# Kernel optimization log

Measured on AMD Instinct MI355X. Metric: run time of the kernel, lower is better.

Reference implementation:

```python
import jax, jax.numpy as jnp
import numpy as np

B, S, D = 2, 2048, 1024
H = 16
HD = D // H
E = 8          # num_experts
TOPK = 2
DF = 4 * D     # expert hidden
LN_EPS = 1e-5


def _layer_norm(h, g, b):
    mu = jnp.mean(h, axis=-1, keepdims=True)
    var = jnp.mean(jnp.square(h - mu), axis=-1, keepdims=True)
    return (h - mu) * jax.lax.rsqrt(var + LN_EPS) * g + b


def setup_inputs() -> dict:
    key = jax.random.key(0)
    ks = jax.random.split(key, 12)
    s = lambda fan: 1.0 / np.sqrt(fan)
    return {
        "x": jax.random.normal(ks[0], (B, S, D), jnp.float32),
        "ln1_g": jnp.ones((D,), jnp.float32),
        "ln1_b": jnp.zeros((D,), jnp.float32),
        "ln2_g": jnp.ones((D,), jnp.float32),
        "ln2_b": jnp.zeros((D,), jnp.float32),
        "wqkv": jax.random.normal(ks[1], (D, 3 * D), jnp.float32) * s(D),
        "bqkv": jnp.zeros((3 * D,), jnp.float32),
        "wo": jax.random.normal(ks[2], (D, D), jnp.float32) * s(D),
        "bo": jnp.zeros((D,), jnp.float32),
        "w_router": jax.random.normal(ks[3], (D, E), jnp.float32) * s(D),
        "w1": jax.random.normal(ks[4], (E, D, DF), jnp.float32) * s(D),
        "b1": jnp.zeros((E, DF), jnp.float32),
        "w2": jax.random.normal(ks[5], (E, DF, D), jnp.float32) * s(DF),
        "b2": jnp.zeros((E, D), jnp.float32),
    }


def reference(x, ln1_g, ln1_b, ln2_g, ln2_b, wqkv, bqkv, wo, bo,
              w_router, w1, b1, w2, b2):
    # ---- pre-norm causal self-attention (dropout = identity in eval) ----
    h = _layer_norm(x, ln1_g, ln1_b)
    qkv = h @ wqkv + bqkv                                  # [B,S,3D]
    qkv = qkv.reshape(B, S, 3, H, HD)
    q, k, v = (jnp.moveaxis(qkv[:, :, i], 1, 2) for i in range(3))  # [B,H,S,HD]
    scores = jnp.einsum("bhqd,bhkd->bhqk", q, k) / np.sqrt(HD)
    causal = jnp.tril(jnp.ones((S, S), bool))
    scores = jnp.where(causal, scores, jnp.finfo(scores.dtype).min)
    attn = jax.nn.softmax(scores, axis=-1)
    ctx = jnp.einsum("bhqk,bhkd->bhqd", attn, v)           # [B,H,S,HD]
    ctx = jnp.moveaxis(ctx, 1, 2).reshape(B, S, D)
    x = x + (ctx @ wo + bo)

    # ---- pre-norm top-2 MoE FFN ----
    h2 = _layer_norm(x, ln2_g, ln2_b)
    t = h2.reshape(B * S, D)                               # tokens [T,D]
    logits = t @ w_router                                  # [T,E]
    probs = jax.nn.softmax(logits, axis=-1)
    top_v, top_i = jax.lax.top_k(probs, TOPK)              # [T,2]
    top_v = top_v / jnp.sum(top_v, axis=-1, keepdims=True)
    # combine gates as dense [T,E] (zero for unselected experts)
    gates = jnp.sum(jax.nn.one_hot(top_i, E, dtype=t.dtype) * top_v[..., None], axis=1)
    # dense all-expert compute, weighted combine (same math as sparse dispatch)
    hid = jax.nn.gelu(jnp.einsum("td,edf->etf", t, w1) + b1[:, None, :], approximate=False)
    eout = jnp.einsum("etf,efd->etd", hid, w2) + b2[:, None, :]   # [E,T,D]
    ffn_out = jnp.einsum("etd,te->td", eout, gates).reshape(B, S, D)

    return x + ffn_out
```

## Files before the change

kernel.cpp:

```cpp
#include <hip/hip_runtime.h>
#include <hip/hip_bf16.h>
#include <math.h>

#define NB    2
#define SEQ   2048
#define DMODEL 1024
#define NH    16
#define HDIM  64
#define NE    8
#define DFF   4096
#define TTOK  4096

#define MT_MAX   72
#define SLOT_MAX 9216

#define C_CNT  0
#define C_FILL 8
#define C_BASE 16
#define C_NMT  24
#define C_MTE  32
#define C_MTS  104

typedef __attribute__((ext_vector_type(8))) short short8;
typedef __attribute__((ext_vector_type(4))) float f32x4;
// ... 61 lines not shown
    unsigned short h1 = f2bf(r[1]); hi.y = h1; lo.y = f2bf(r[1] - bf2f(h1));
    unsigned short h2 = f2bf(r[2]); hi.z = h2; lo.z = f2bf(r[2] - bf2f(h2));
    unsigned short h3 = f2bf(r[3]); hi.w = h3; lo.w = f2bf(r[3] - bf2f(h3));
    ((ushort4*)(outb  + (size_t)t * DMODEL))[tid] = hi;
    ((ushort4*)(outlo + (size_t)t * DMODEL))[tid] = lo;
  }
}

template<int EPI>
__global__ __launch_bounds__(256) void mgemm_split(
    const unsigned short* __restrict__ Ah,
    const unsigned short* __restrict__ Alo,
    const unsigned short* __restrict__ Bth,
    const unsigned short* __restrict__ Btl,
    const float* __restrict__ bias,
    const float* __restrict__ resid,
    float* __restrict__ C, int M, int N, int K)
{
  __shared__ unsigned short AH[128][32];
  __shared__ unsigned short AL[128][32];
  __shared__ unsigned short BH[128][32];
  __shared__ unsigned short BL[128][32];
  int tid = threadIdx.x;
  int l = tid & 63, wv = tid >> 6;
  int wr = wv >> 1, wc = wv & 1;
  int m0 = blockIdx.y * 128, n0 = blockIdx.x * 128;
  int rsub = l >> 2, csub = (l & 3) * 8;
  int row0 = wv * 32 + rsub, row1 = row0 + 16;

  const unsigned short* gah0 = Ah  + (size_t)(m0 + row0) * K + csub;
  const unsigned short* gah1 = Ah  + (size_t)(m0 + row1) * K + csub;
  const unsigned short* gal0 = Alo + (size_t)(m0 + row0) * K + csub;
  const unsigned short* gal1 = Alo + (size_t)(m0 + row1) * K + csub;
  const unsigned short* gbh0 = Bth + (size_t)(n0 + row0) * K + csub;
  const unsigned short* gbh1 = Bth + (size_t)(n0 + row1) * K + csub;
  const unsigned short* gbl0 = Btl + (size_t)(n0 + row0) * K + csub;
  const unsigned short* gbl1 = Btl + (size_t)(n0 + row1) * K + csub;

  const f32x4 z = {0.f, 0.f, 0.f, 0.f};
  f32x4 acc[4][4];
  #pragma unroll
  for (int i = 0; i < 4; ++i)
    #pragma unroll
    for (int j = 0; j < 4; ++j) acc[i][j] = z;

  for (int k0 = 0; k0 < K; k0 += 32) {
    __syncthreads();
    gl_lds16(gah0 + k0, &AH[wv * 32][0]);
    gl_lds16(gah1 + k0, &AH[wv * 32 + 16][0]);
    gl_lds16(gal0 + k0, &AL[wv * 32][0]);
    gl_lds16(gal1 + k0, &AL[wv * 32 + 16][0]);
    gl_lds16(gbh0 + k0, &BH[wv * 32][0]);
    gl_lds16(gbh1 + k0, &BH[wv * 32 + 16][0]);
    gl_lds16(gbl0 + k0, &BL[wv * 32][0]);
    gl_lds16(gbl1 + k0, &BL[wv * 32 + 16][0]);
    __syncthreads();

    short8 afh[4], afl[4], bfh[4], bfl[4];
    #pragma unroll
    for (int m = 0; m < 4; ++m) {
      afh[m] = *(const short8*)(&AH[wr * 64 + m * 16 + (l & 15)][(l >> 4) << 3]);
      afl[m] = *(const short8*)(&AL[wr * 64 + m * 16 + (l & 15)][(l >> 4) << 3]);
    }
    #pragma unroll
    for (int n = 0; n < 4; ++n) {
      bfh[n] = *(const short8*)(&BH[wc * 64 + n * 16 + (l & 15)][(l >> 4) << 3]);
      bfl[n] = *(const short8*)(&BL[wc * 64 + n * 16 + (l & 15)][(l >> 4) << 3]);
    }
    #pragma unroll
    for (int m = 0; m < 4; ++m)
      #pragma unroll
      for (int n = 0; n < 4; ++n) {
        acc[m][n] = __builtin_amdgcn_mfma_f32_16x16x32_bf16(afh[m], bfh[n], acc[m][n], 0, 0, 0);
        acc[m][n] = __builtin_amdgcn_mfma_f32_16x16x32_bf16(afl[m], bfh[n], acc[m][n], 0, 0, 0);
        acc[m][n] = __builtin_amdgcn_mfma_f32_16x16x32_bf16(afh[m], bfl[n], acc[m][n], 0, 0, 0);
      }
  }

  int rbase = m0 + wr * 64 + ((l >> 4) << 2);
  int cbase = n0 + wc * 64 + (l & 15);
  #pragma unroll
  for (int n = 0; n < 4; ++n) {
    int col = cbase + n * 16;
    float bv = bias[col];
    #pragma unroll
    for (int m = 0; m < 4; ++m) {
      #pragma unroll
      for (int r = 0; r < 4; ++r) {
        int row = rbase + m * 16 + r;
        float v = acc[m][n][r] + bv;
        if constexpr (EPI == 1) v += resid[(size_t)row * N + col];
        C[(size_t)row * N + col] = v;
      }
    }
  }
}

__global__ __launch_bounds__(256) void qkv_split(
    const float* __restrict__ qkv,
    unsigned short* __restrict__ Qh, unsigned short* __restrict__ Ql,
    unsigned short* __restrict__ Kh, unsigned short* __restrict__ Kl,
    unsigned short* __restrict__ Vth, unsigned short* __restrict__ Vtl)
{
  __shared__ float Vt[64][68];
  int st = blockIdx.x, bh = blockIdx.y;
  int b = bh >> 4, h = bh & 15;
  int tid = threadIdx.x;
  int row = tid >> 2, cs = (tid & 3) * 16;
  size_t hb = (size_t)bh * SEQ * 64;
  int srow = st * 64 + row;
  size_t src = (size_t)(b * SEQ + srow) * 3072 + (size_t)h * HDIM + cs;

  #pragma unroll
  for (int qk = 0; qk < 2; ++qk) {
    const float* p = qkv + src + qk * 1024;
    unsigned short hi8[16], lo8[16];
    #pragma unroll
    for (int i = 0; i < 16; ++i) {
      float v = p[i];
      unsigned short hh_ = f2bf(v);
      hi8[i] = hh_; lo8[i] = f2bf(v - bf2f(hh_));
    }
    unsigned short* dh = (qk ? Kh : Qh) + hb + (size_t)srow * 64 + cs;
    unsigned short* dl = (qk ? Kl : Ql) + hb + (size_t)srow * 64 + cs;
    *(uint4v*)dh       = *(const uint4v*)&hi8[0];
    *(uint4v*)(dh + 8) = *(const uint4v*)&hi8[8];
    *(uint4v*)dl       = *(const uint4v*)&lo8[0];
    *(uint4v*)(dl + 8) = *(const uint4v*)&lo8[8];
  }
  {
    const float* p = qkv + src + 2048;
    #pragma unroll
    for (int i = 0; i < 4; ++i)
      *(f32x4*)&Vt[row][cs + i * 4] = *(const f32x4*)(p + i * 4);
  }
  __syncthreads();
  {
    int d = tid >> 2, ks = (tid & 3) * 16;
    unsigned short hi8[16], lo8[16];
    #pragma unroll
    for (int j = 0; j < 16; ++j) {
      float v = Vt[ks + j][d];
      unsigned short hh_ = f2bf(v);
      hi8[j] = hh_; lo8[j] = f2bf(v - bf2f(hh_));
    }
    size_t dst = hb + (size_t)d * SEQ + st * 64 + ks;
    *(uint4v*)(Vth + dst)     = *(const uint4v*)&hi8[0];
    *(uint4v*)(Vth + dst + 8) = *(const uint4v*)&hi8[8];
    *(uint4v*)(Vtl + dst)     = *(const uint4v*)&lo8[0];
    *(uint4v*)(Vtl + dst + 8) = *(const uint4v*)&lo8[8];
  }
}

__global__ __launch_bounds__(256) void attn_mf(
    const unsigned short* __restrict__ Qh, const unsigned short* __restrict__ Ql,
    const unsigned short* __restrict__ Kh, const unsigned short* __restrict__ Kl,
    const unsigned short* __restrict__ Vth, const unsigned short* __restrict__ Vtl,
    unsigned short* __restrict__ ctxh, unsigned short* __restrict__ ctxl)
{
  __shared__ unsigned short KVh[64][72], KVl[64][72];
  __shared__ unsigned short Phs[64][72], Pls[64][72];
  int bh = blockIdx.y;
  int b = bh >> 4, h = bh & 15;
  int bx = blockIdx.x;
  int qt = (bx & 1) ? (31 - (bx >> 1)) : (bx >> 1);
  int tid = threadIdx.x, wv = tid >> 6, l = tid & 63;
  int lm = l & 15, lh = l >> 4;
  const size_t hb = (size_t)bh * SEQ * 64;
  int q0 = qt * 64 + wv * 16;

  short8 aQh[2], aQl[2];
  {
    size_t qa = hb + (size_t)(q0 + lm) * 64 + (lh << 3);
    aQh[0] = *(const short8*)(Qh + qa);
    aQh[1] = *(const short8*)(Qh + qa + 32);
    aQl[0] = *(const short8*)(Ql + qa);
    aQl[1] = *(const short8*)(Ql + qa + 32);
  }
  const f32x4 z = {0.f, 0.f, 0.f, 0.f};
  f32x4 ctx[4] = {z, z, z, z};
  float mrun[4] = {-1e4f, -1e4f, -1e4f, -1e4f};
  float lrun[4] = {0.f, 0.f, 0.f, 0.f};

  int srow = tid >> 2, scs = (tid & 3) * 16;
  for (int kt = 0; kt <= qt; ++kt) {
    uint4v vh0, vh1, vl0, vl1;
    {
      size_t vg = hb + (size_t)srow * SEQ + kt * 64 + scs;
      vh0 = *(const uint4v*)(Vth + vg);
      vh1 = *(const uint4v*)(Vth + vg + 8);
      vl0 = *(const uint4v*)(Vtl + vg);
      vl1 = *(const uint4v*)(Vtl + vg + 8);
    }
    __syncthreads();
    {
      size_t kg = hb + (size_t)(kt * 64 + srow) * 64 + scs;
      *(uint4v*)&KVh[srow][scs]     = *(const uint4v*)(Kh + kg);
      *(uint4v*)&KVh[srow][scs + 8] = *(const uint4v*)(Kh + kg + 8);
      *(uint4v*)&KVl[srow][scs]     = *(const uint4v*)(Kl + kg);
      *(uint4v*)&KVl[srow][scs + 8] = *(const uint4v*)(Kl + kg + 8);
    }
    __syncthreads();

    f32x4 S4[4] = {z, z, z, z};
    #pragma unroll
    for (int n = 0; n < 4; ++n) {
      #pragma unroll
      for (int c = 0; c < 2; ++c) {
        short8 kbh = *(const short8*)&KVh[n * 16 + lm][c * 32 + (lh << 3)];
        short8 kbl = *(const short8*)&KVl[n * 16 + lm][c * 32 + (lh << 3)];
        S4[n] = __builtin_amdgcn_mfma_f32_16x16x32_bf16(aQh[c], kbh, S4[n], 0, 0, 0);
        S4[n] = __builtin_amdgcn_mfma_f32_16x16x32_bf16(aQl[c], kbh, S4[n], 0, 0, 0);
        S4[n] = __builtin_amdgcn_mfma_f32_16x16x32_bf16(aQh[c], kbl, S4[n], 0, 0, 0);
      }
    }
    bool diag = (kt == qt);
    int qin = wv * 16 + lh * 4;
    #pragma unroll
    for (int r = 0; r < 4; ++r) {
      float s0 = S4[0][r] * 0.125f, s1 = S4[1][r] * 0.125f;
      float s2 = S4[2][r] * 0.125f, s3 = S4[3][r] * 0.125f;
      if (diag) {
        int qq = qin + r;
        if (lm      > qq) s0 = -1e30f;
        if (16 + lm > qq) s1 = -1e30f;
        if (32 + lm > qq) s2 = -1e30f;
        if (48 + lm > qq) s3 = -1e30f;
      }
      float cm = fmaxf(fmaxf(s0, s1), fmaxf(s2, s3));
      cm = fmaxf(cm, __shfl_xor(cm, 1));
      cm = fmaxf(cm, __shfl_xor(cm, 2));
      cm = fmaxf(cm, __shfl_xor(cm, 4));
      cm = fmaxf(cm, __shfl_xor(cm, 8));
      if (cm > mrun[r] + 8.0f) {
        float sc = __expf(mrun[r] - cm);
        lrun[r] *= sc;
        ctx[0][r] *= sc; ctx[1][r] *= sc; ctx[2][r] *= sc; ctx[3][r] *= sc;
        mrun[r] = cm;
      }
      float p0 = __expf(s0 - mrun[r]), p1 = __expf(s1 - mrun[r]);
      float p2 = __expf(s2 - mrun[r]), p3 = __expf(s3 - mrun[r]);
      float rs = (p0 + p1) + (p2 + p3);
      rs += __shfl_xor(rs, 1); rs += __shfl_xor(rs, 2);
      rs += __shfl_xor(rs, 4); rs += __shfl_xor(rs, 8);
      lrun[r] += rs;
      int prow = qin + r;
      unsigned short e0 = f2bf(p0); Phs[prow][lm]      = e0; Pls[prow][lm]      = f2bf(p0 - bf2f(e0));
      unsigned short e1 = f2bf(p1); Phs[prow][16 + lm] = e1; Pls[prow][16 + lm] = f2bf(p1 - bf2f(e1));
      unsigned short e2 = f2bf(p2); Phs[prow][32 + lm] = e2; Pls[prow][32 + lm] = f2bf(p2 - bf2f(e2));
      unsigned short e3 = f2bf(p3); Phs[prow][48 + lm] = e3; Pls[prow][48 + lm] = f2bf(p3 - bf2f(e3));
    }
    __syncthreads();
    {
      *(uint4v*)&KVh[srow][scs]     = vh0;
      *(uint4v*)&KVh[srow][scs + 8] = vh1;
      *(uint4v*)&KVl[srow][scs]     = vl0;
      *(uint4v*)&KVl[srow][scs + 8] = vl1;
    }
    __syncthreads();

    #pragma unroll
    for (int c = 0; c < 2; ++c) {
      short8 pah = *(const short8*)&Phs[wv * 16 + lm][c * 32 + (lh << 3)];
      short8 pal = *(const short8*)&Pls[wv * 16 + lm][c * 32 + (lh << 3)];
      #pragma unroll
      for (int n = 0; n < 4; ++n) {
        short8 vbh = *(const short8*)&KVh[n * 16 + lm][c * 32 + (lh << 3)];
        short8 vbl = *(const short8*)&KVl[n * 16 + lm][c * 32 + (lh << 3)];
        ctx[n] = __builtin_amdgcn_mfma_f32_16x16x32_bf16(pah, vbh, ctx[n], 0, 0, 0);
        ctx[n] = __builtin_amdgcn_mfma_f32_16x16x32_bf16(pal, vbh, ctx[n], 0, 0, 0);
        ctx[n] = __builtin_amdgcn_mfma_f32_16x16x32_bf16(pah, vbl, ctx[n], 0, 0, 0);
      }
    }
  }

  #pragma unroll
  for (int r = 0; r < 4; ++r) {
    float inv = 1.0f / lrun[r];
    int qg = b * SEQ + qt * 64 + wv * 16 + lh * 4 + r;
    size_t ob = (size_t)qg * DMODEL + (size_t)h * HDIM + lm;
    #pragma unroll
    for (int n = 0; n < 4; ++n) {
      float v = ctx[n][r] * inv;
      unsigned short hi = f2bf(v);
      ctxh[ob + n * 16] = hi;
      ctxl[ob + n * 16] = f2bf(v - bf2f(hi));
    }
  }
}

__global__ __launch_bounds__(256) void router_kernel(
    const float* __restrict__ x1,
    const float* __restrict__ gam,
    const float* __restrict__ bet,
    const float* __restrict__ wrt,
    int* __restrict__ ctrl,
    int2* __restrict__ t_e,
    float2* __restrict__ t_g)
{
  int w = threadIdx.x >> 6, l = threadIdx.x & 63;
  int t = blockIdx.x * 4 + w;
  const f32x4* row = (const f32x4*)(x1 + (size_t)t * DMODEL);
  f32x4 v[4];
  float s = 0.f, sq = 0.f;
  #pragma unroll
  for (int i = 0; i < 4; ++i) {
    v[i] = row[l + i * 64];
    #pragma unroll
    for (int j = 0; j < 4; ++j) { s += v[i][j]; sq += v[i][j] * v[i][j]; }
  }
  #pragma unroll
  for (int off = 1; off < 64; off <<= 1) {
    s  += __shfl_xor(s, off);
    sq += __shfl_xor(sq, off);
  }
  float mu  = s * (1.0f / DMODEL);
  float var = sq * (1.0f / DMODEL) - mu * mu;
  float rs  = rsqrtf(var + 1e-5f);

  float acc[NE] = {0.f, 0.f, 0.f, 0.f, 0.f, 0.f, 0.f, 0.f};
  #pragma unroll
  for (int i = 0; i < 4; ++i) {
    int base = (l + i * 64) * 4;
    #pragma unroll
    for (int j = 0; j < 4; ++j) {
      int idx = base + j;
      float xn = (v[i][j] - mu) * rs * gam[idx] + bet[idx];
      const f32x4* wr0 = (const f32x4*)(wrt + idx * NE);
      f32x4 w0 = wr0[0], w1v = wr0[1];
      acc[0] += xn * w0[0]; acc[1] += xn * w0[1];
      acc[2] += xn * w0[2]; acc[3] += xn * w0[3];
      acc[4] += xn * w1v[0]; acc[5] += xn * w1v[1];
      acc[6] += xn * w1v[2]; acc[7] += xn * w1v[3];
    }
  }
  #pragma unroll
  for (int e = 0; e < NE; ++e) {
    #pragma unroll
    for (int off = 1; off < 64; off <<= 1) acc[e] += __shfl_xor(acc[e], off);
  }
  if (l == 0) {
    int e0 = 0; float m0v = acc[0];
    #pragma unroll
    for (int e = 1; e < NE; ++e) if (acc[e] > m0v) { m0v = acc[e]; e0 = e; }
    int e1 = -1; float m1v = -1e30f;
    #pragma unroll
    for (int e = 0; e < NE; ++e) if (e != e0 && acc[e] > m1v) { m1v = acc[e]; e1 = e; }
    float r = __expf(m1v - m0v);
    float g0 = 1.0f / (1.0f + r);
    float g1 = r * g0;
    t_e[t] = make_int2(e0, e1);
    t_g[t] = make_float2(g0, g1);
    atomicAdd(&ctrl[C_CNT + e0], 1);
    atomicAdd(&ctrl[C_CNT + e1], 1);
  }
}

__global__ void scan_kernel(int* __restrict__ ctrl)
{
  if (threadIdx.x == 0 && blockIdx.x == 0) {
    int b = 0, m = 0;
    for (int e = 0; e < NE; ++e) {
      ctrl[C_BASE + e] = b;
      int pc = (ctrl[C_CNT + e] + 127) & ~127;
      int nt = pc >> 7;
      for (int i = 0; i < nt; ++i) {
        ctrl[C_MTE + m] = e;
        ctrl[C_MTS + m] = b + (i << 7);
        ++m;
      }
      b += pc;
    }
    ctrl[C_NMT] = m;
  }
}

__global__ __launch_bounds__(256) void gather_kernel(
    int* __restrict__ ctrl,
    const int2* __restrict__ t_e,
    const float2* __restrict__ t_g,
    int* __restrict__ slot_token,
    float* __restrict__ slot_gate)
{
  int t = blockIdx.x * 256 + threadIdx.x;
  int2 e = t_e[t];
  float2 g = t_g[t];
  int p0 = atomicAdd(&ctrl[C_FILL + e.x], 1);
  int s0 = ctrl[C_BASE + e.x] + p0;
  slot_token[s0] = t; slot_gate[s0] = g.x;
  int p1 = atomicAdd(&ctrl[C_FILL + e.y], 1);
  int s1 = ctrl[C_BASE + e.y] + p1;
  slot_token[s1] = t; slot_gate[s1] = g.y;
}

__global__ __launch_bounds__(256) void transpose_conv(
    const float* __restrict__ in, unsigned short* __restrict__ outb,
    unsigned short* __restrict__ outlo, int K, int N)
{
  __shared__ float T[64][68];
  int e = blockIdx.z;
  int n0 = blockIdx.x * 64, k0 = blockIdx.y * 64;
  const float* src = in + (size_t)e * K * N;
  unsigned short* dst = outb + (size_t)e * K * N;
  unsigned short* dstl = outlo ? outlo + (size_t)e * K * N : nullptr;
  int tid = threadIdx.x;
  int r = tid >> 4, c4 = (tid & 15) * 4;
  #pragma unroll
  for (int i = 0; i < 4; ++i) {
    f32x4 v = *(const f32x4*)(src + (size_t)(k0 + r + i * 16) * N + n0 + c4);
    *(f32x4*)(&T[r + i * 16][c4]) = v;
  }
  __syncthreads();
  #pragma unroll
  for (int i = 0; i < 4; ++i) {
    int rr = r + i * 16;
    float v0 = T[c4 + 0][rr], v1 = T[c4 + 1][rr];
    float v2 = T[c4 + 2][rr], v3 = T[c4 + 3][rr];
    ushort4 o;
    o.x = f2bf(v0); o.y = f2bf(v1); o.z = f2bf(v2); o.w = f2bf(v3);
    *(ushort4*)(dst + (size_t)(n0 + rr) * K + k0 + c4) = o;
    if (dstl) {
      ushort4 lo;
      lo.x = f2bf(v0 - bf2f(o.x));
      lo.y = f2bf(v1 - bf2f(o.y));
      lo.z = f2bf(v2 - bf2f(o.z));
      lo.w = f2bf(v3 - bf2f(o.w));
      *(ushort4*)(dstl + (size_t)(n0 + rr) * K + k0 + c4) = lo;
    }
  }
}

__global__ __launch_bounds__(256) void moe_w1f(
    const unsigned short* __restrict__ h2,
    const unsigned short* __restrict__ w1t,
    const float* __restrict__ b1,
    const int* __restrict__ ctrl,
    const int* __restrict__ slot_token,
    unsigned short* __restrict__ Hs)
{
  int mt = blockIdx.y;
  if (mt >= ctrl[C_NMT]) return;
// ... 69 lines not shown
    }
  }
}

__global__ __launch_bounds__(256) void moe_w2f(
    const unsigned short* __restrict__ Hs,
    const unsigned short* __restrict__ w2t,
    const float* __restrict__ b2,
    const int* __restrict__ ctrl,
    const int* __restrict__ slot_token,
    const float* __restrict__ slot_gate,
    float* __restrict__ ffn)
{
  int mt = blockIdx.y;
  if (mt >= ctrl[C_NMT]) return;
  int e = ctrl[C_MTE + mt];
  int slot0 = ctrl[C_MTS + mt];
  const int N = DMODEL, K = DFF;
  const unsigned short* Bt = w2t + (size_t)e * (size_t)K * N;
  const float* bias = b2 + (size_t)e * DMODEL;

  __shared__ unsigned short Al[128][32];
  __shared__ unsigned short Bl[128][32];
  int tid = threadIdx.x;
  int l = tid & 63, wv = tid >> 6;
  int wr = wv >> 1, wc = wv & 1;
  int n0 = blockIdx.x * 128;
  int rsub = l >> 2, csub = (l & 3) * 8;
  int row0 = wv * 32 + rsub, row1 = row0 + 16;
  const unsigned short* ga0 = Hs + (size_t)(slot0 + row0) * DFF + csub;
  const unsigned short* ga1 = Hs + (size_t)(slot0 + row1) * DFF + csub;
  const unsigned short* gb0 = Bt + (size_t)(n0 + row0) * K + csub;
  const unsigned short* gb1 = Bt + (size_t)(n0 + row1) * K + csub;

  const f32x4 z = {0.f, 0.f, 0.f, 0.f};
  f32x4 acc[4][4];
  #pragma unroll
  for (int i = 0; i < 4; ++i)
    #pragma unroll
    for (int j = 0; j < 4; ++j) acc[i][j] = z;

  for (int k0 = 0; k0 < K; k0 += 32) {
    __syncthreads();
    gl_lds16(ga0 + k0, &Al[wv * 32][0]);
    gl_lds16(ga1 + k0, &Al[wv * 32 + 16][0]);
    gl_lds16(gb0 + k0, &Bl[wv * 32][0]);
    gl_lds16(gb1 + k0, &Bl[wv * 32 + 16][0]);
    __syncthreads();

    short8 af[4], bfr[4];
    #pragma unroll
    for (int m = 0; m < 4; ++m)
      af[m] = *(const short8*)(&Al[wr * 64 + m * 16 + (l & 15)][(l >> 4) << 3]);
    #pragma unroll
    for (int n = 0; n < 4; ++n)
      bfr[n] = *(const short8*)(&Bl[wc * 64 + n * 16 + (l & 15)][(l >> 4) << 3]);
    #pragma unroll
    for (int m = 0; m < 4; ++m)
      #pragma unroll
      for (int n = 0; n < 4; ++n)
        acc[m][n] = __builtin_amdgcn_mfma_f32_16x16x32_bf16(af[m], bfr[n], acc[m][n], 0, 0, 0);
  }

  int rbase = wr * 64 + ((l >> 4) << 2);
  int cbase = n0 + wc * 64 + (l & 15);
  #pragma unroll
  for (int n = 0; n < 4; ++n) {
    int col = cbase + n * 16;
    float bv = bias[col];
    #pragma unroll
    for (int m = 0; m < 4; ++m) {
      #pragma unroll
      for (int r = 0; r < 4; ++r) {
        int srow = slot0 + rbase + m * 16 + r;
        int tok = slot_token[srow];
        if (tok >= 0) {
          float v = acc[m][n][r] + bv;
          atomicAdd(&ffn[(size_t)tok * DMODEL + col], slot_gate[srow] * v);
        }
      }
    }
  }
}

__global__ __launch_bounds__(256) void final_add(
    const float* __restrict__ x1,
    const float* __restrict__ ffn,
    float* __restrict__ out)
{
  int i = blockIdx.x * 256 + threadIdx.x;
  f32x4 xr = ((const f32x4*)x1)[i];
  f32x4 fr = ((const f32x4*)ffn)[i];
  f32x4 o;
  o[0] = xr[0] + fr[0];
  o[1] = xr[1] + fr[1];
  o[2] = xr[2] + fr[2];
  o[3] = xr[3] + fr[3];
  ((f32x4*)out)[i] = o;
}

extern "C" void kernel_launch(void* const* d_in, const int* in_sizes, int n_in,
                              void* d_out, int out_size, void* d_ws, size_t ws_size,
                              hipStream_t stream) {
  (void)in_sizes; (void)n_in; (void)out_size;
  const float* x     = (const float*)d_in[0];
  const float* ln1_g = (const float*)d_in[1];
  const float* ln1_b = (const float*)d_in[2];
  const float* ln2_g = (const float*)d_in[3];
  const float* ln2_b = (const float*)d_in[4];
  const float* wqkv  = (const float*)d_in[5];
  const float* bqkv  = (const float*)d_in[6];
  const float* wo    = (const float*)d_in[7];
  const float* bo    = (const float*)d_in[8];
  const float* wrt   = (const float*)d_in[9];
  const float* w1    = (const float*)d_in[10];
  const float* b1    = (const float*)d_in[11];
  const float* w2    = (const float*)d_in[12];
  const float* b2    = (const float*)d_in[13];
  float* out = (float*)d_out;

  char* ws = (char*)d_ws;
  size_t off = 0;
  auto alloc = [&](size_t bytes) -> void* {
    void* p = ws + off;
    off += (bytes + 255) & ~(size_t)255;
    return p;
  };
  float*          x1    = (float*)alloc((size_t)TTOK * DMODEL * 4);
  unsigned short* h2    = (unsigned short*)alloc((size_t)TTOK * DMODEL * 2);
  int*            ctrl  = (int*)alloc(1024);
  int2*           t_e   = (int2*)alloc((size_t)TTOK * 8);
  float2*         t_g   = (float2*)alloc((size_t)TTOK * 8);
  int*            slot_token = (int*)alloc((size_t)SLOT_MAX * 4);
  float*          slot_gate  = (float*)alloc((size_t)SLOT_MAX * 4);
  float*          P1    = (float*)alloc((size_t)TTOK * DMODEL * 4);
  char*           P2    = (char*)alloc((size_t)SLOT_MAX * DFF * 2);
  unsigned short* w1t   = (unsigned short*)alloc((size_t)NE * DMODEL * DFF * 2);
  unsigned short* w2t   = (unsigned short*)alloc((size_t)NE * DFF * DMODEL * 2);
  unsigned short* wqkvTh = (unsigned short*)alloc((size_t)DMODEL * 3 * DMODEL * 2);
  unsigned short* wqkvTl = (unsigned short*)alloc((size_t)DMODEL * 3 * DMODEL * 2);
  unsigned short* woTh  = (unsigned short*)alloc((size_t)DMODEL * DMODEL * 2);
  unsigned short* woTl  = (unsigned short*)alloc((size_t)DMODEL * DMODEL * 2);
  unsigned short* hh    = (unsigned short*)alloc((size_t)TTOK * DMODEL * 2);
  unsigned short* hl    = (unsigned short*)alloc((size_t)TTOK * DMODEL * 2);
  unsigned short* ctxh  = (unsigned short*)alloc((size_t)TTOK * DMODEL * 2);
  unsigned short* ctxl  = (unsigned short*)alloc((size_t)TTOK * DMODEL * 2);
  size_t headsz = (size_t)NB * NH * SEQ * HDIM;
  unsigned short* Qh  = (unsigned short*)alloc(headsz * 2);
  unsigned short* Ql  = (unsigned short*)alloc(headsz * 2);
  unsigned short* Khp = (unsigned short*)alloc(headsz * 2);
  unsigned short* Klp = (unsigned short*)alloc(headsz * 2);
  unsigned short* Vth = (unsigned short*)alloc(headsz * 2);
  unsigned short* Vtl = (unsigned short*)alloc(headsz * 2);

  float*          qkv  = (float*)P2;
  float*          ffn  = P1;
  unsigned short* Hs   = (unsigned short*)P2;

  hipMemsetAsync(ctrl, 0, 16 * 4, stream);
  hipMemsetAsync(slot_token, 0xFF, (size_t)SLOT_MAX * 4, stream);

  transpose_conv<<<dim3(DFF / 64, DMODEL / 64, NE), 256, 0, stream>>>(
      w1, w1t, nullptr, DMODEL, DFF);
  transpose_conv<<<dim3(DMODEL / 64, DFF / 64, NE), 256, 0, stream>>>(
      w2, w2t, nullptr, DFF, DMODEL);
  transpose_conv<<<dim3(3 * DMODEL / 64, DMODEL / 64, 1), 256, 0, stream>>>(
      wqkv, wqkvTh, wqkvTl, DMODEL, 3 * DMODEL);
  transpose_conv<<<dim3(DMODEL / 64, DMODEL / 64, 1), 256, 0, stream>>>(
      wo, woTh, woTl, DMODEL, DMODEL);

  ln_kernel<2><<<TTOK, 256, 0, stream>>>(x, ln1_g, ln1_b, nullptr, hh, hl);
  mgemm_split<0><<<dim3(3 * DMODEL / 128, TTOK / 128), 256, 0, stream>>>(
      hh, hl, wqkvTh, wqkvTl, bqkv, nullptr, qkv, TTOK, 3 * DMODEL, DMODEL);
  qkv_split<<<dim3(SEQ / 64, NB * NH), 256, 0, stream>>>(
      qkv, Qh, Ql, Khp, Klp, Vth, Vtl);
  attn_mf<<<dim3(32, NB * NH), 256, 0, stream>>>(
      Qh, Ql, Khp, Klp, Vth, Vtl, ctxh, ctxl);
  mgemm_split<1><<<dim3(DMODEL / 128, TTOK / 128), 256, 0, stream>>>(
      ctxh, ctxl, woTh, woTl, bo, x, x1, TTOK, DMODEL, DMODEL);

  ln_kernel<1><<<TTOK, 256, 0, stream>>>(x1, ln2_g, ln2_b, nullptr, h2, nullptr);
  router_kernel<<<TTOK / 4, 256, 0, stream>>>(x1, ln2_g, ln2_b, wrt, ctrl, t_e, t_g);
  scan_kernel<<<1, 64, 0, stream>>>(ctrl);
  gather_kernel<<<TTOK / 256, 256, 0, stream>>>(ctrl, t_e, t_g, slot_token, slot_gate);
  hipMemsetAsync(ffn, 0, (size_t)TTOK * DMODEL * 4, stream);
  moe_w1f<<<dim3(DFF / 128, MT_MAX), 256, 0, stream>>>(
      h2, w1t, b1, ctrl, slot_token, Hs);
  moe_w2f<<<dim3(DMODEL / 128, MT_MAX), 256, 0, stream>>>(
      Hs, w2t, b2, ctrl, slot_token, slot_gate, ffn);
  final_add<<<(TTOK * DMODEL / 4) / 256, 256, 0, stream>>>(x1, ffn, out);
}
```

Measured before the change: 980.1 us.

## Pair complementary causal query tiles per attention block to share K/V loads

Each attention workgroup now handles two query tiles, p and 31-p, walking the K/V tiles once and reusing each staged K/V tile for both. This balances causal work across blocks and halves K/V global reads for the shorter tile's range. The cost is half as many blocks (512 instead of 1024), twice the register state (two Q fragments, accumulators and softmax stats) and extra LDS for a second P buffer, which may lower occupancy.

```diff
diff --git a/kernel.cpp b/kernel.cpp
--- a/kernel.cpp
+++ b/kernel.cpp
@@ -237,38 +237,42 @@
   }
 }
 
-__global__ __launch_bounds__(256) void attn_mf(
+__global__ __launch_bounds__(256) void attn_mf2(
     const unsigned short* __restrict__ Qh, const unsigned short* __restrict__ Ql,
     const unsigned short* __restrict__ Kh, const unsigned short* __restrict__ Kl,
     const unsigned short* __restrict__ Vth, const unsigned short* __restrict__ Vtl,
     unsigned short* __restrict__ ctxh, unsigned short* __restrict__ ctxl)
 {
   __shared__ unsigned short KVh[64][72], KVl[64][72];
-  __shared__ unsigned short Phs[64][72], Pls[64][72];
+  __shared__ unsigned short PAh[64][72], PAl[64][72];
+  __shared__ unsigned short PBh[64][72], PBl[64][72];
   int bh = blockIdx.y;
   int b = bh >> 4, h = bh & 15;
-  int bx = blockIdx.x;
-  int qt = (bx & 1) ? (31 - (bx >> 1)) : (bx >> 1);
+  int p = blockIdx.x;
+  int qtA = p, qtB = 31 - p;
   int tid = threadIdx.x, wv = tid >> 6, l = tid & 63;
   int lm = l & 15, lh = l >> 4;
   const size_t hb = (size_t)bh * SEQ * 64;
-  int q0 = qt * 64 + wv * 16;
-
-  short8 aQh[2], aQl[2];
+
+  short8 aQAh[2], aQAl[2], aQBh[2], aQBl[2];
   {
-    size_t qa = hb + (size_t)(q0 + lm) * 64 + (lh << 3);
-    aQh[0] = *(const short8*)(Qh + qa);
-    aQh[1] = *(const short8*)(Qh + qa + 32);
-    aQl[0] = *(const short8*)(Ql + qa);
-    aQl[1] = *(const short8*)(Ql + qa + 32);
+    size_t qa = hb + (size_t)(qtA * 64 + wv * 16 + lm) * 64 + (lh << 3);
+    size_t qb = hb + (size_t)(qtB * 64 + wv * 16 + lm) * 64 + (lh << 3);
+    aQAh[0] = *(const short8*)(Qh + qa); aQAh[1] = *(const short8*)(Qh + qa + 32);
+    aQAl[0] = *(const short8*)(Ql + qa); aQAl[1] = *(const short8*)(Ql + qa + 32);
+    aQBh[0] = *(const short8*)(Qh + qb); aQBh[1] = *(const short8*)(Qh + qb + 32);
+    aQBl[0] = *(const short8*)(Ql + qb); aQBl[1] = *(const short8*)(Ql + qb + 32);
   }
   const f32x4 z = {0.f, 0.f, 0.f, 0.f};
-  f32x4 ctx[4] = {z, z, z, z};
-  float mrun[4] = {-1e4f, -1e4f, -1e4f, -1e4f};
-  float lrun[4] = {0.f, 0.f, 0.f, 0.f};
+  f32x4 ctxA[4] = {z, z, z, z}, ctxB[4] = {z, z, z, z};
+  float mA[4] = {-1e4f, -1e4f, -1e4f, -1e4f}, lA[4] = {0.f, 0.f, 0.f, 0.f};
+  float mB[4] = {-1e4f, -1e4f, -1e4f, -1e4f}, lB[4] = {0.f, 0.f, 0.f, 0.f};
 
   int srow = tid >> 2, scs = (tid & 3) * 16;
-  for (int kt = 0; kt <= qt; ++kt) {
+  int qin = wv * 16 + lh * 4;
+
+  for (int kt = 0; kt <= qtB; ++kt) {
+    bool actA = (kt <= qtA);
     uint4v vh0, vh1, vl0, vl1;
     {
       size_t vg = hb + (size_t)srow * SEQ + kt * 64 + scs;
@@ -287,25 +291,29 @@
     }
     __syncthreads();
 
-    f32x4 S4[4] = {z, z, z, z};
+    f32x4 SA[4] = {z, z, z, z}, SB[4] = {z, z, z, z};
     #pragma unroll
     for (int n = 0; n < 4; ++n) {
       #pragma unroll
       for (int c = 0; c < 2; ++c) {
         short8 kbh = *(const short8*)&KVh[n * 16 + lm][c * 32 + (lh << 3)];
         short8 kbl = *(const short8*)&KVl[n * 16 + lm][c * 32 + (lh << 3)];
-        S4[n] = __builtin_amdgcn_mfma_f32_16x16x32_bf16(aQh[c], kbh, S4[n], 0, 0, 0);
-        S4[n] = __builtin_amdgcn_mfma_f32_16x16x32_bf16(aQl[c], kbh, S4[n], 0, 0, 0);
-        S4[n] = __builtin_amdgcn_mfma_f32_16x16x32_bf16(aQh[c], kbl, S4[n], 0, 0, 0);
-      }
-    }
-    bool diag = (kt == qt);
-    int qin = wv * 16 + lh * 4;
+        SB[n] = __builtin_amdgcn_mfma_f32_16x16x32_bf16(aQBh[c], kbh, SB[n], 0, 0, 0);
+        SB[n] = __builtin_amdgcn_mfma_f32_16x16x32_bf16(aQBl[c], kbh, SB[n], 0, 0, 0);
+        SB[n] = __builtin_amdgcn_mfma_f32_16x16x32_bf16(aQBh[c], kbl, SB[n], 0, 0, 0);
+        if (actA) {
+          SA[n] = __builtin_amdgcn_mfma_f32_16x16x32_bf16(aQAh[c], kbh, SA[n], 0, 0, 0);
+          SA[n] = __builtin_amdgcn_mfma_f32_16x16x32_bf16(aQAl[c], kbh, SA[n], 0, 0, 0);
+          SA[n] = __builtin_amdgcn_mfma_f32_16x16x32_bf16(aQAh[c], kbl, SA[n], 0, 0, 0);
+        }
+      }
+    }
+    bool diagB = (kt == qtB);
     #pragma unroll
     for (int r = 0; r < 4; ++r) {
-      float s0 = S4[0][r] * 0.125f, s1 = S4[1][r] * 0.125f;
-      float s2 = S4[2][r] * 0.125f, s3 = S4[3][r] * 0.125f;
-      if (diag) {
+      float s0 = SB[0][r] * 0.125f, s1 = SB[1][r] * 0.125f;
+      float s2 = SB[2][r] * 0.125f, s3 = SB[3][r] * 0.125f;
+      if (diagB) {
         int qq = qin + r;
         if (lm      > qq) s0 = -1e30f;
         if (16 + lm > qq) s1 = -1e30f;
@@ -317,23 +325,60 @@
       cm = fmaxf(cm, __shfl_xor(cm, 2));
       cm = fmaxf(cm, __shfl_xor(cm, 4));
       cm = fmaxf(cm, __shfl_xor(cm, 8));
-      if (cm > mrun[r] + 8.0f) {
-        float sc = __expf(mrun[r] - cm);
-        lrun[r] *= sc;
-        ctx[0][r] *= sc; ctx[1][r] *= sc; ctx[2][r] *= sc; ctx[3][r] *= sc;
-        mrun[r] = cm;
-      }
-      float p0 = __expf(s0 - mrun[r]), p1 = __expf(s1 - mrun[r]);
-      float p2 = __expf(s2 - mrun[r]), p3 = __expf(s3 - mrun[r]);
+      if (cm > mB[r] + 8.0f) {
+        float sc = __expf(mB[r] - cm);
+        lB[r] *= sc;
+        ctxB[0][r] *= sc; ctxB[1][r] *= sc; ctxB[2][r] *= sc; ctxB[3][r] *= sc;
+        mB[r] = cm;
+      }
+      float p0 = __expf(s0 - mB[r]), p1 = __expf(s1 - mB[r]);
+      float p2 = __expf(s2 - mB[r]), p3 = __expf(s3 - mB[r]);
       float rs = (p0 + p1) + (p2 + p3);
       rs += __shfl_xor(rs, 1); rs += __shfl_xor(rs, 2);
       rs += __shfl_xor(rs, 4); rs += __shfl_xor(rs, 8);
-      lrun[r] += rs;
+      lB[r] += rs;
       int prow = qin + r;
-      unsigned short e0 = f2bf(p0); Phs[prow][lm]      = e0; Pls[prow][lm]      = f2bf(p0 - bf2f(e0));
-      unsigned short e1 = f2bf(p1); Phs[prow][16 + lm] = e1; Pls[prow][16 + lm] = f2bf(p1 - bf2f(e1));
-      unsigned short e2 = f2bf(p2); Phs[prow][32 + lm] = e2; Pls[prow][32 + lm] = f2bf(p2 - bf2f(e2));
-      unsigned short e3 = f2bf(p3); Phs[prow][48 + lm] = e3; Pls[prow][48 + lm] = f2bf(p3 - bf2f(e3));
+      unsigned short e0 = f2bf(p0); PBh[prow][lm]      = e0; PBl[prow][lm]      = f2bf(p0 - bf2f(e0));
+      unsigned short e1 = f2bf(p1); PBh[prow][16 + lm] = e1; PBl[prow][16 + lm] = f2bf(p1 - bf2f(e1));
+      unsigned short e2 = f2bf(p2); PBh[prow][32 + lm] = e2; PBl[prow][32 + lm] = f2bf(p2 - bf2f(e2));
+      unsigned short e3 = f2bf(p3); PBh[prow][48 + lm] = e3; PBl[prow][48 + lm] = f2bf(p3 - bf2f(e3));
+    }
+    if (actA) {
+      bool diagA = (kt == qtA);
+      #pragma unroll
+      for (int r = 0; r < 4; ++r) {
+        float s0 = SA[0][r] * 0.125f, s1 = SA[1][r] * 0.125f;
+        float s2 = SA[2][r] * 0.125f, s3 = SA[3][r] * 0.125f;
+        if (diagA) {
+          int qq = qin + r;
+          if (lm      > qq) s0 = -1e30f;
+          if (16 + lm > qq) s1 = -1e30f;
+          if (32 + lm > qq) s2 = -1e30f;
+          if (48 + lm > qq) s3 = -1e30f;
+        }
+        float cm = fmaxf(fmaxf(s0, s1), fmaxf(s2, s3));
+        cm = fmaxf(cm, __shfl_xor(cm, 1));
+        cm = fmaxf(cm, __shfl_xor(cm, 2));
+        cm = fmaxf(cm, __shfl_xor(cm, 4));
+        cm = fmaxf(cm, __shfl_xor(cm, 8));
+        if (cm > mA[r] + 8.0f) {
+          float sc = __expf(mA[r] - cm);
+          lA[r] *= sc;
+          ctxA[0][r] *= sc; ctxA[1][r] *= sc; ctxA[2][r] *= sc; ctxA[3][r] *= sc;
+          mA[r] = cm;
+        }
+        float p0 = __expf(s0 - mA[r]), p1 = __expf(s1 - mA[r]);
+        float p2 = __expf(s2 - mA[r]), p3 = __expf(s3 - mA[r]);
+        float rs = (p0 + p1) + (p2 + p3);
+        rs += __shfl_xor(rs, 1); rs += __shfl_xor(rs, 2);
+        rs += __shfl_xor(rs, 4); rs += __shfl_xor(rs, 8);
+        lA[r] += rs;
+        int prow = qin + r;
+        unsigned short e0 = f2bf(p0); PAh[prow][lm]      = e0; PAl[prow][lm]      = f2bf(p0 - bf2f(e0));
+        unsigned short e1 = f2bf(p1); PAh[prow][16 + lm] = e1; PAl[prow][16 + lm] = f2bf(p1 - bf2f(e1));
+        unsigned short e2 = f2bf(p2); PAh[prow][32 + lm] = e2; PAl[prow][32 + lm] = f2bf(p2 - bf2f(e2));
+        unsigned short e3 = f2bf(p3); PAh[prow][48 + lm] = e3; PAl[prow][48 + lm] = f2bf(p3 - bf2f(e3));
+      }
     }
     __syncthreads();
     {
@@ -346,32 +391,46 @@
 
     #pragma unroll
     for (int c = 0; c < 2; ++c) {
-      short8 pah = *(const short8*)&Phs[wv * 16 + lm][c * 32 + (lh << 3)];
-      short8 pal = *(const short8*)&Pls[wv * 16 + lm][c * 32 + (lh << 3)];
+      short8 pbh = *(const short8*)&PBh[wv * 16 + lm][c * 32 + (lh << 3)];
+      short8 pbl = *(const short8*)&PBl[wv * 16 + lm][c * 32 + (lh << 3)];
+      short8 pah, pal;
+      if (actA) {
+        pah = *(const short8*)&PAh[wv * 16 + lm][c * 32 + (lh << 3)];
+        pal = *(const short8*)&PAl[wv * 16 + lm][c * 32 + (lh << 3)];
+      }
       #pragma unroll
       for (int n = 0; n < 4; ++n) {
         short8 vbh = *(const short8*)&KVh[n * 16 + lm][c * 32 + (lh << 3)];
         short8 vbl = *(const short8*)&KVl[n * 16 + lm][c * 32 + (lh << 3)];
-        ctx[n] = __builtin_amdgcn_mfma_f32_16x16x32_bf16(pah, vbh, ctx[n], 0, 0, 0);
-        ctx[n] = __builtin_amdgcn_mfma_f32_16x16x32_bf16(pal, vbh, ctx[n], 0, 0, 0);
-        ctx[n] = __builtin_amdgcn_mfma_f32_16x16x32_bf16(pah, vbl, ctx[n], 0, 0, 0);
-      }
-    }
-  }
-
-  #pragma unroll
-  for (int r = 0; r < 4; ++r) {
-    float inv = 1.0f / lrun[r];
-    int qg = b * SEQ + qt * 64 + wv * 16 + lh * 4 + r;
-    size_t ob = (size_t)qg * DMODEL + (size_t)h * HDIM + lm;
-    #pragma unroll
-    for (int n = 0; n < 4; ++n) {
-      float v = ctx[n][r] * inv;
-      unsigned short hi = f2bf(v);
-      ctxh[ob + n * 16] = hi;
-      ctxl[ob + n * 16] = f2bf(v - bf2f(hi));
-    }
-  }
+        ctxB[n] = __builtin_amdgcn_mfma_f32_16x16x32_bf16(pbh, vbh, ctxB[n], 0, 0, 0);
+        ctxB[n] = __builtin_amdgcn_mfma_f32_16x16x32_bf16(pbl, vbh, ctxB[n], 0, 0, 0);
+        ctxB[n] = __builtin_amdgcn_mfma_f32_16x16x32_bf16(pbh, vbl, ctxB[n], 0, 0, 0);
+        if (actA) {
+          ctxA[n] = __builtin_amdgcn_mfma_f32_16x16x32_bf16(pah, vbh, ctxA[n], 0, 0, 0);
+          ctxA[n] = __builtin_amdgcn_mfma_f32_16x16x32_bf16(pal, vbh, ctxA[n], 0, 0, 0);
+          ctxA[n] = __builtin_amdgcn_mfma_f32_16x16x32_bf16(pah, vbl, ctxA[n], 0, 0, 0);
+        }
+      }
+    }
+  }
+
+  auto wout = [&](int qt, f32x4* ctx, float* lrun) {
+    #pragma unroll
+    for (int r = 0; r < 4; ++r) {
+      float inv = 1.0f / lrun[r];
+      int qg = b * SEQ + qt * 64 + wv * 16 + lh * 4 + r;
+      size_t ob = (size_t)qg * DMODEL + (size_t)h * HDIM + lm;
+      #pragma unroll
+      for (int n = 0; n < 4; ++n) {
+        float v = ctx[n][r] * inv;
+        unsigned short hi = f2bf(v);
+        ctxh[ob + n * 16] = hi;
+        ctxl[ob + n * 16] = f2bf(v - bf2f(hi));
+      }
+    }
+  };
+  wout(qtA, ctxA, lA);
+  wout(qtB, ctxB, lB);
 }
 
 __global__ __launch_bounds__(256) void router_kernel(
@@ -769,7 +828,7 @@
       hh, hl, wqkvTh, wqkvTl, bqkv, nullptr, qkv, TTOK, 3 * DMODEL, DMODEL);
   qkv_split<<<dim3(SEQ / 64, NB * NH), 256, 0, stream>>>(
       qkv, Qh, Ql, Khp, Klp, Vth, Vtl);
-  attn_mf<<<dim3(32, NB * NH), 256, 0, stream>>>(
+  attn_mf2<<<dim3(16, NB * NH), 256, 0, stream>>>(
       Qh, Ql, Khp, Klp, Vth, Vtl, ctxh, ctxl);
   mgemm_split<1><<<dim3(DMODEL / 128, TTOK / 128), 256, 0, stream>>>(
       ctxh, ctxl, woTh, woTl, bo, x, x1, TTOK, DMODEL, DMODEL);
```

Measured after the change: 992.9 us. No clear change (+1.3%).

## Split attention KV range across two blocks with paired query tiles and merge

Applied to the files above, without the earlier changes.

Each attention block now handles two query tiles (p and 31-p) and processes only every other KV tile (split by parity), writing unnormalized fp32 partial outputs plus running max and sum. A new merge kernel combines the two parity partials with log-sum-exp rescaling and emits the bf16 hi/lo context. This balances causal work per block and raises parallelism per query tile, at the cost of extra fp32 partial traffic and an additional kernel launch.

```diff
diff --git a/kernel.cpp b/kernel.cpp
--- a/kernel.cpp
+++ b/kernel.cpp
@@ -237,140 +237,187 @@
   }
 }
 
-__global__ __launch_bounds__(256) void attn_mf(
+__global__ __launch_bounds__(256) void attn_mf3(
     const unsigned short* __restrict__ Qh, const unsigned short* __restrict__ Ql,
     const unsigned short* __restrict__ Kh, const unsigned short* __restrict__ Kl,
     const unsigned short* __restrict__ Vth, const unsigned short* __restrict__ Vtl,
-    unsigned short* __restrict__ ctxh, unsigned short* __restrict__ ctxl)
+    float* __restrict__ paro,
+    float* __restrict__ parml)
 {
   __shared__ unsigned short KVh[64][72], KVl[64][72];
   __shared__ unsigned short Phs[64][72], Pls[64][72];
   int bh = blockIdx.y;
   int b = bh >> 4, h = bh & 15;
   int bx = blockIdx.x;
-  int qt = (bx & 1) ? (31 - (bx >> 1)) : (bx >> 1);
+  int p  = bx >> 1, par = bx & 1;
   int tid = threadIdx.x, wv = tid >> 6, l = tid & 63;
   int lm = l & 15, lh = l >> 4;
   const size_t hb = (size_t)bh * SEQ * 64;
-  int q0 = qt * 64 + wv * 16;
-
-  short8 aQh[2], aQl[2];
-  {
-    size_t qa = hb + (size_t)(q0 + lm) * 64 + (lh << 3);
-    aQh[0] = *(const short8*)(Qh + qa);
-    aQh[1] = *(const short8*)(Qh + qa + 32);
-    aQl[0] = *(const short8*)(Ql + qa);
-    aQl[1] = *(const short8*)(Ql + qa + 32);
-  }
+  int srow = tid >> 2, scs = (tid & 3) * 16;
+  int qin = wv * 16 + lh * 4;
   const f32x4 z = {0.f, 0.f, 0.f, 0.f};
-  f32x4 ctx[4] = {z, z, z, z};
-  float mrun[4] = {-1e4f, -1e4f, -1e4f, -1e4f};
-  float lrun[4] = {0.f, 0.f, 0.f, 0.f};
-
-  int srow = tid >> 2, scs = (tid & 3) * 16;
-  for (int kt = 0; kt <= qt; ++kt) {
-    uint4v vh0, vh1, vl0, vl1;
+
+  #pragma unroll 1
+  for (int job = 0; job < 2; ++job) {
+    int qt = job ? (31 - p) : p;
+    int q0 = qt * 64 + wv * 16;
+
+    short8 aQh[2], aQl[2];
     {
-      size_t vg = hb + (size_t)srow * SEQ + kt * 64 + scs;
-      vh0 = *(const uint4v*)(Vth + vg);
-      vh1 = *(const uint4v*)(Vth + vg + 8);
-      vl0 = *(const uint4v*)(Vtl + vg);
-      vl1 = *(const uint4v*)(Vtl + vg + 8);
-    }
-    __syncthreads();
-    {
-      size_t kg = hb + (size_t)(kt * 64 + srow) * 64 + scs;
-      *(uint4v*)&KVh[srow][scs]     = *(const uint4v*)(Kh + kg);
-      *(uint4v*)&KVh[srow][scs + 8] = *(const uint4v*)(Kh + kg + 8);
-      *(uint4v*)&KVl[srow][scs]     = *(const uint4v*)(Kl + kg);
-      *(uint4v*)&KVl[srow][scs + 8] = *(const uint4v*)(Kl + kg + 8);
-    }
-    __syncthreads();
-
-    f32x4 S4[4] = {z, z, z, z};
-    #pragma unroll
-    for (int n = 0; n < 4; ++n) {
+      size_t qa = hb + (size_t)(q0 + lm) * 64 + (lh << 3);
+      aQh[0] = *(const short8*)(Qh + qa);
+      aQh[1] = *(const short8*)(Qh + qa + 32);
+      aQl[0] = *(const short8*)(Ql + qa);
+      aQl[1] = *(const short8*)(Ql + qa + 32);
+    }
+    f32x4 ctx[4] = {z, z, z, z};
+    float mrun[4] = {-1e4f, -1e4f, -1e4f, -1e4f};
+    float lrun[4] = {0.f, 0.f, 0.f, 0.f};
+
+    for (int kt = par; kt <= qt; kt += 2) {
+      uint4v vh0, vh1, vl0, vl1;
+      {
+        size_t vg = hb + (size_t)srow * SEQ + kt * 64 + scs;
+        vh0 = *(const uint4v*)(Vth + vg);
+        vh1 = *(const uint4v*)(Vth + vg + 8);
+        vl0 = *(const uint4v*)(Vtl + vg);
+        vl1 = *(const uint4v*)(Vtl + vg + 8);
+      }
+      __syncthreads();
+      {
+        size_t kg = hb + (size_t)(kt * 64 + srow) * 64 + scs;
+        *(uint4v*)&KVh[srow][scs]     = *(const uint4v*)(Kh + kg);
+        *(uint4v*)&KVh[srow][scs + 8] = *(const uint4v*)(Kh + kg + 8);
+        *(uint4v*)&KVl[srow][scs]     = *(const uint4v*)(Kl + kg);
+        *(uint4v*)&KVl[srow][scs + 8] = *(const uint4v*)(Kl + kg + 8);
+      }
+      __syncthreads();
+
+      f32x4 S4[4] = {z, z, z, z};
+      #pragma unroll
+      for (int n = 0; n < 4; ++n) {
+        #pragma unroll
+        for (int c = 0; c < 2; ++c) {
+          short8 kbh = *(const short8*)&KVh[n * 16 + lm][c * 32 + (lh << 3)];
+          short8 kbl = *(const short8*)&KVl[n * 16 + lm][c * 32 + (lh << 3)];
+          S4[n] = __builtin_amdgcn_mfma_f32_16x16x32_bf16(aQh[c], kbh, S4[n], 0, 0, 0);
+          S4[n] = __builtin_amdgcn_mfma_f32_16x16x32_bf16(aQl[c], kbh, S4[n], 0, 0, 0);
+          S4[n] = __builtin_amdgcn_mfma_f32_16x16x32_bf16(aQh[c], kbl, S4[n], 0, 0, 0);
+        }
+      }
+      bool diag = (kt == qt);
+      #pragma unroll
+      for (int r = 0; r < 4; ++r) {
+        float s0 = S4[0][r] * 0.125f, s1 = S4[1][r] * 0.125f;
+        float s2 = S4[2][r] * 0.125f, s3 = S4[3][r] * 0.125f;
+        if (diag) {
+          int qq = qin + r;
+          if (lm      > qq) s0 = -1e30f;
+          if (16 + lm > qq) s1 = -1e30f;
+          if (32 + lm > qq) s2 = -1e30f;
+          if (48 + lm > qq) s3 = -1e30f;
+        }
+        float cm = fmaxf(fmaxf(s0, s1), fmaxf(s2, s3));
+        cm = fmaxf(cm, __shfl_xor(cm, 1));
+        cm = fmaxf(cm, __shfl_xor(cm, 2));
+        cm = fmaxf(cm, __shfl_xor(cm, 4));
+        cm = fmaxf(cm, __shfl_xor(cm, 8));
+        if (cm > mrun[r] + 8.0f) {
+          float sc = __expf(mrun[r] - cm);
+          lrun[r] *= sc;
+          ctx[0][r] *= sc; ctx[1][r] *= sc; ctx[2][r] *= sc; ctx[3][r] *= sc;
+          mrun[r] = cm;
+        }
+        float p0 = __expf(s0 - mrun[r]), p1 = __expf(s1 - mrun[r]);
+        float p2 = __expf(s2 - mrun[r]), p3 = __expf(s3 - mrun[r]);
+        float rs = (p0 + p1) + (p2 + p3);
+        rs += __shfl_xor(rs, 1); rs += __shfl_xor(rs, 2);
+        rs += __shfl_xor(rs, 4); rs += __shfl_xor(rs, 8);
+        lrun[r] += rs;
+        int prow = qin + r;
+        unsigned short e0 = f2bf(p0); Phs[prow][lm]      = e0; Pls[prow][lm]      = f2bf(p0 - bf2f(e0));
+        unsigned short e1 = f2bf(p1); Phs[prow][16 + lm] = e1; Pls[prow][16 + lm] = f2bf(p1 - bf2f(e1));
+        unsigned short e2 = f2bf(p2); Phs[prow][32 + lm] = e2; Pls[prow][32 + lm] = f2bf(p2 - bf2f(e2));
+        unsigned short e3 = f2bf(p3); Phs[prow][48 + lm] = e3; Pls[prow][48 + lm] = f2bf(p3 - bf2f(e3));
+      }
+      __syncthreads();
+      {
+        *(uint4v*)&KVh[srow][scs]     = vh0;
+        *(uint4v*)&KVh[srow][scs + 8] = vh1;
+        *(uint4v*)&KVl[srow][scs]     = vl0;
+        *(uint4v*)&KVl[srow][scs + 8] = vl1;
+      }
+      __syncthreads();
+
       #pragma unroll
       for (int c = 0; c < 2; ++c) {
-        short8 kbh = *(const short8*)&KVh[n * 16 + lm][c * 32 + (lh << 3)];
-        short8 kbl = *(const short8*)&KVl[n * 16 + lm][c * 32 + (lh << 3)];
-        S4[n] = __builtin_amdgcn_mfma_f32_16x16x32_bf16(aQh[c], kbh, S4[n], 0, 0, 0);
-        S4[n] = __builtin_amdgcn_mfma_f32_16x16x32_bf16(aQl[c], kbh, S4[n], 0, 0, 0);
-        S4[n] = __builtin_amdgcn_mfma_f32_16x16x32_bf16(aQh[c], kbl, S4[n], 0, 0, 0);
-      }
-    }
-    bool diag = (kt == qt);
-    int qin = wv * 16 + lh * 4;
+        short8 pah = *(const short8*)&Phs[wv * 16 + lm][c * 32 + (lh << 3)];
+        short8 pal = *(const short8*)&Pls[wv * 16 + lm][c * 32 + (lh << 3)];
+        #pragma unroll
+        for (int n = 0; n < 4; ++n) {
+          short8 vbh = *(const short8*)&KVh[n * 16 + lm][c * 32 + (lh << 3)];
+          short8 vbl = *(const short8*)&KVl[n * 16 + lm][c * 32 + (lh << 3)];
+          ctx[n] = __builtin_amdgcn_mfma_f32_16x16x32_bf16(pah, vbh, ctx[n], 0, 0, 0);
+          ctx[n] = __builtin_amdgcn_mfma_f32_16x16x32_bf16(pal, vbh, ctx[n], 0, 0, 0);
+          ctx[n] = __builtin_amdgcn_mfma_f32_16x16x32_bf16(pah, vbl, ctx[n], 0, 0, 0);
+        }
+      }
+    }
+
     #pragma unroll
     for (int r = 0; r < 4; ++r) {
-      float s0 = S4[0][r] * 0.125f, s1 = S4[1][r] * 0.125f;
-      float s2 = S4[2][r] * 0.125f, s3 = S4[3][r] * 0.125f;
-      if (diag) {
-        int qq = qin + r;
-        if (lm      > qq) s0 = -1e30f;
-        if (16 + lm > qq) s1 = -1e30f;
-        if (32 + lm > qq) s2 = -1e30f;
-        if (48 + lm > qq) s3 = -1e30f;
-      }
-      float cm = fmaxf(fmaxf(s0, s1), fmaxf(s2, s3));
-      cm = fmaxf(cm, __shfl_xor(cm, 1));
-      cm = fmaxf(cm, __shfl_xor(cm, 2));
-      cm = fmaxf(cm, __shfl_xor(cm, 4));
-      cm = fmaxf(cm, __shfl_xor(cm, 8));
-      if (cm > mrun[r] + 8.0f) {
-        float sc = __expf(mrun[r] - cm);
-        lrun[r] *= sc;
-        ctx[0][r] *= sc; ctx[1][r] *= sc; ctx[2][r] *= sc; ctx[3][r] *= sc;
-        mrun[r] = cm;
-      }
-      float p0 = __expf(s0 - mrun[r]), p1 = __expf(s1 - mrun[r]);
-      float p2 = __expf(s2 - mrun[r]), p3 = __expf(s3 - mrun[r]);
-      float rs = (p0 + p1) + (p2 + p3);
-      rs += __shfl_xor(rs, 1); rs += __shfl_xor(rs, 2);
-      rs += __shfl_xor(rs, 4); rs += __shfl_xor(rs, 8);
-      lrun[r] += rs;
-      int prow = qin + r;
-      unsigned short e0 = f2bf(p0); Phs[prow][lm]      = e0; Pls[prow][lm]      = f2bf(p0 - bf2f(e0));
-      unsigned short e1 = f2bf(p1); Phs[prow][16 + lm] = e1; Pls[prow][16 + lm] = f2bf(p1 - bf2f(e1));
-      unsigned short e2 = f2bf(p2); Phs[prow][32 + lm] = e2; Pls[prow][32 + lm] = f2bf(p2 - bf2f(e2));
-      unsigned short e3 = f2bf(p3); Phs[prow][48 + lm] = e3; Pls[prow][48 + lm] = f2bf(p3 - bf2f(e3));
-    }
-    __syncthreads();
-    {
-      *(uint4v*)&KVh[srow][scs]     = vh0;
-      *(uint4v*)&KVh[srow][scs + 8] = vh1;
-      *(uint4v*)&KVl[srow][scs]     = vl0;
-      *(uint4v*)&KVl[srow][scs + 8] = vl1;
-    }
-    __syncthreads();
-
-    #pragma unroll
-    for (int c = 0; c < 2; ++c) {
-      short8 pah = *(const short8*)&Phs[wv * 16 + lm][c * 32 + (lh << 3)];
-      short8 pal = *(const short8*)&Pls[wv * 16 + lm][c * 32 + (lh << 3)];
-      #pragma unroll
-      for (int n = 0; n < 4; ++n) {
-        short8 vbh = *(const short8*)&KVh[n * 16 + lm][c * 32 + (lh << 3)];
-        short8 vbl = *(const short8*)&KVl[n * 16 + lm][c * 32 + (lh << 3)];
-        ctx[n] = __builtin_amdgcn_mfma_f32_16x16x32_bf16(pah, vbh, ctx[n], 0, 0, 0);
-        ctx[n] = __builtin_amdgcn_mfma_f32_16x16x32_bf16(pal, vbh, ctx[n], 0, 0, 0);
-        ctx[n] = __builtin_amdgcn_mfma_f32_16x16x32_bf16(pah, vbl, ctx[n], 0, 0, 0);
-      }
-    }
-  }
-
-  #pragma unroll
-  for (int r = 0; r < 4; ++r) {
-    float inv = 1.0f / lrun[r];
-    int qg = b * SEQ + qt * 64 + wv * 16 + lh * 4 + r;
-    size_t ob = (size_t)qg * DMODEL + (size_t)h * HDIM + lm;
-    #pragma unroll
-    for (int n = 0; n < 4; ++n) {
-      float v = ctx[n][r] * inv;
-      unsigned short hi = f2bf(v);
-      ctxh[ob + n * 16] = hi;
-      ctxl[ob + n * 16] = f2bf(v - bf2f(hi));
-    }
+      int qg = b * SEQ + qt * 64 + wv * 16 + lh * 4 + r;
+      size_t ob = ((size_t)par * TTOK + qg) * DMODEL + (size_t)h * HDIM + lm;
+      #pragma unroll
+      for (int n = 0; n < 4; ++n) paro[ob + n * 16] = ctx[n][r];
+      if (lm == 0) {
+        size_t mb = (((size_t)par * TTOK + qg) * NH + h) * 2;
+        parml[mb] = mrun[r]; parml[mb + 1] = lrun[r];
+      }
+    }
+  }
+}
+
+template<int NS>
+__global__ __launch_bounds__(256) void attn_merge(
+    const float* __restrict__ paro,
+    const float* __restrict__ parml,
+    unsigned short* __restrict__ ctxh,
+    unsigned short* __restrict__ ctxl)
+{
+  int gid = blockIdx.x * 256 + threadIdx.x;
+  int ds = gid & 3;
+  int h  = (gid >> 2) & 15;
+  int t  = gid >> 6;
+  float m[NS], lv[NS];
+  float mx = -1e30f;
+  #pragma unroll
+  for (int i = 0; i < NS; ++i) {
+    size_t mb = (((size_t)i * TTOK + t) * NH + h) * 2;
+    m[i] = parml[mb]; lv[i] = parml[mb + 1];
+    mx = fmaxf(mx, m[i]);
+  }
+  float w[NS], lsum = 0.f;
+  #pragma unroll
+  for (int i = 0; i < NS; ++i) { w[i] = __expf(m[i] - mx); lsum += lv[i] * w[i]; }
+  float inv = 1.0f / lsum;
+  size_t ob = (size_t)t * DMODEL + (size_t)h * HDIM + ds * 16;
+  #pragma unroll
+  for (int i4 = 0; i4 < 4; ++i4) {
+    f32x4 v = {0.f, 0.f, 0.f, 0.f};
+    #pragma unroll
+    for (int i = 0; i < NS; ++i) {
+      const f32x4* oi = (const f32x4*)(paro + (size_t)i * TTOK * DMODEL + ob);
+      v += oi[i4] * w[i];
+    }
+    v = v * inv;
+    ushort4 hi, lo;
+    unsigned short e0 = f2bf(v[0]); hi.x = e0; lo.x = f2bf(v[0] - bf2f(e0));
+    unsigned short e1 = f2bf(v[1]); hi.y = e1; lo.y = f2bf(v[1] - bf2f(e1));
+    unsigned short e2 = f2bf(v[2]); hi.z = e2; lo.z = f2bf(v[2] - bf2f(e2));
+    unsigned short e3 = f2bf(v[3]); hi.w = e3; lo.w = f2bf(v[3] - bf2f(e3));
+    *(ushort4*)(ctxh + ob + i4 * 4) = hi;
+    *(ushort4*)(ctxl + ob + i4 * 4) = lo;
   }
 }
 
@@ -747,6 +794,8 @@
   unsigned short* Klp = (unsigned short*)alloc(headsz * 2);
   unsigned short* Vth = (unsigned short*)alloc(headsz * 2);
   unsigned short* Vtl = (unsigned short*)alloc(headsz * 2);
+  float*          paro2  = (float*)alloc((size_t)2 * TTOK * DMODEL * 4);
+  float*          parml2 = (float*)alloc((size_t)2 * TTOK * NH * 2 * 4);
 
   float*          qkv  = (float*)P2;
   float*          ffn  = P1;
@@ -769,8 +818,10 @@
       hh, hl, wqkvTh, wqkvTl, bqkv, nullptr, qkv, TTOK, 3 * DMODEL, DMODEL);
   qkv_split<<<dim3(SEQ / 64, NB * NH), 256, 0, stream>>>(
       qkv, Qh, Ql, Khp, Klp, Vth, Vtl);
-  attn_mf<<<dim3(32, NB * NH), 256, 0, stream>>>(
-      Qh, Ql, Khp, Klp, Vth, Vtl, ctxh, ctxl);
+  attn_mf3<<<dim3(32, NB * NH), 256, 0, stream>>>(
+      Qh, Ql, Khp, Klp, Vth, Vtl, paro2, parml2);
+  attn_merge<2><<<(TTOK * NH * 4) / 256, 256, 0, stream>>>(
+      paro2, parml2, ctxh, ctxl);
   mgemm_split<1><<<dim3(DMODEL / 128, TTOK / 128), 256, 0, stream>>>(
       ctxh, ctxl, woTh, woTl, bo, x, x1, TTOK, DMODEL, DMODEL);
 
```

Measured after the change: 902.3 us (median of 2 runs). 1.09x faster.
